# Kernel optimization log

Hardware: AMD Instinct MI355X
Metric: run time of the kernel (lower is better)

## Reference

```python
import jax, jax.numpy as jnp
import numpy as np

# BiAttn: additive (concat-based) cross attention.
# Original torch: e = Linear([k_i ; q_j]) = k_i @ W[:H] + q_j @ W[H:] + b  (separable)
# a = softmax(e, axis=-1 over Y); out[b,x,h] = sum_y v[b,y,h] * a[b,x,y]

B, X, Y, H = 8, 2048, 2048, 1024


def setup_inputs() -> dict:
    key = jax.random.key(0)
    kq, kk, kv, kw = jax.random.split(key, 4)
    q = jax.random.normal(kq, (B, Y, H), dtype=jnp.float32)
    k = jax.random.normal(kk, (B, X, H), dtype=jnp.float32)
    v = jax.random.normal(kv, (B, Y, H), dtype=jnp.float32)
    W = jax.random.normal(kw, (2 * H,), dtype=jnp.float32) * (1.0 / np.sqrt(2 * H))
    b = jnp.zeros((), dtype=jnp.float32)
    return {"q": q, "k": k, "v": v, "W": W, "b": b}


def reference(q, k, v, W, b):
    Hdim = k.shape[-1]
    Wk, Wq = W[:Hdim], W[Hdim:]
    # Separable additive score: e[b,x,y] = k[b,x]@Wk + q[b,y]@Wq + b
    sk = jnp.einsum('bxh,h->bx', k, Wk)          # [B, X]
    sq = jnp.einsum('byh,h->by', q, Wq)          # [B, Y]
    e = sk[:, :, None] + sq[:, None, :] + b      # [B, X, Y]
    a = jax.nn.softmax(e, axis=-1)               # softmax over Y
    out = jnp.einsum('byh,bxy->bxh', v, a)       # [B, X, H]
    return out
```

## Files before the change

### kernel.cpp

```cpp
#include <hip/hip_runtime.h>

#define Bn 8
#define Xn 2048
#define Yn 2048
#define Hn 1024
#define RPB 8
#define NPB (Yn / RPB)
#define YC 64
#define NCH (Yn / YC)


__global__ __launch_bounds__(256)
void k_pe(const float* __restrict__ q, const float* __restrict__ W,
          float* __restrict__ pe, float* __restrict__ sb,
          float* __restrict__ o) {
    const int blk = blockIdx.x;
    const int t = threadIdx.x;
    const int wave = t >> 6, lane = t & 63;
    __shared__ float ps[RPB];

    if (t == 0) ((float4*)o)[blk] = make_float4(0.f, 0.f, 0.f, 0.f);

    const float4* w4 = (const float4*)(W + Hn);
    const float4 ww0 = w4[lane];
    const float4 ww1 = w4[lane + 64];
    const float4 ww2 = w4[lane + 128];
    const float4 ww3 = w4[lane + 192];

    const int ra = blk * RPB + wave * 2;
    const float4* qa = (const float4*)(q + (size_t)ra * Hn);
    const float4* qb = qa + (Hn / 4);
    float acca = 0.f, accb = 0.f;
    #pragma unroll
    for (int i = 0; i < 4; ++i) {
        float4 a  = qa[lane + 64 * i];
        float4 bb = qb[lane + 64 * i];
        float4 w  = (i == 0) ? ww0 : (i == 1) ? ww1 : (i == 2) ? ww2 : ww3;
        acca += a.x * w.x + a.y * w.y + a.z * w.z + a.w * w.w;
        accb += bb.x * w.x + bb.y * w.y + bb.z * w.z + bb.w * w.w;
    }
    #pragma unroll
    for (int off = 32; off > 0; off >>= 1) {
        acca += __shfl_xor(acca, off, 64);
        accb += __shfl_xor(accb, off, 64);
    }
    if (lane == 0) {
        float ea = __expf(acca), eb = __expf(accb);
        pe[ra] = ea; pe[ra + 1] = eb;
        ps[wave * 2] = ea; ps[wave * 2 + 1] = eb;
    }
    __syncthreads();
    if (t == 0) {
        float s = 0.f;
        #pragma unroll
        for (int i = 0; i < RPB; ++i) s += ps[i];
        sb[blk] = s;
    }
}

__global__ __launch_bounds__(256)
void k_pv(const float* __restrict__ v, const float* __restrict__ pe,
          const float* __restrict__ sb, float* __restrict__ o) {
    const int b = blockIdx.y;
    const int c = blockIdx.x;
    const int y0 = c * YC;
    const int t = threadIdx.x;
    const int wave = t >> 6, lane = t & 63;
    __shared__ float wred[4];
    __shared__ float pw[YC];

    float s = sb[b * NPB + t];
    #pragma unroll
    for (int off = 32; off > 0; off >>= 1) s += __shfl_xor(s, off, 64);
    if (lane == 0) wred[wave] = s;
    __syncthreads();
    const float inv = 1.f / (wred[0] + wred[1] + wred[2] + wred[3]);

    if (t < YC) pw[t] = pe[b * Yn + y0 + t] * inv;
    __syncthreads();

    const float4* v4 = (const float4*)(v + ((size_t)b * Yn + y0) * Hn);
    float4 acc = {0.f, 0.f, 0.f, 0.f};
    #pragma unroll 16
    for (int yy = 0; yy < YC; ++yy) {
        const float p = pw[yy];
        const float4 vv = v4[(size_t)yy * (Hn / 4) + t];
        acc.x = fmaf(p, vv.x, acc.x);
        acc.y = fmaf(p, vv.y, acc.y);
        acc.z = fmaf(p, vv.z, acc.z);
        acc.w = fmaf(p, vv.w, acc.w);
    }
    float* ob = o + b * Hn + 4 * t;
    atomicAdd(ob + 0, acc.x);
    atomicAdd(ob + 1, acc.y);
    atomicAdd(ob + 2, acc.z);
    atomicAdd(ob + 3, acc.w);
}

__global__ void k_bcast(const float* __restrict__ o, float4* __restrict__ out) {
    const size_t i = (size_t)blockIdx.x * blockDim.x + threadIdx.x;
    const int h4 = (int)(i & (Hn / 4 - 1));
    const size_t row = i >> 8;
    const int b = (int)(row >> 11);
    const float4* o4 = (const float4*)o;
    out[i] = o4[b * (Hn / 4) + h4];
}

extern "C" void kernel_launch(void* const* d_in, const int* in_sizes, int n_in,
                              void* d_out, int out_size, void* d_ws, size_t ws_size,
                              hipStream_t stream) {
    const float* q = (const float*)d_in[0];
    const float* v = (const float*)d_in[2];
    const float* W = (const float*)d_in[3];
    float* out = (float*)d_out;

    float* pe = (float*)d_ws;
    float* sb = pe + (size_t)Bn * Yn;
    float* o  = sb + Bn * NPB;

    k_pe   <<<Bn * Yn / RPB, 256, 0, stream>>>(q, W, pe, sb, o);
    k_pv   <<<dim3(NCH, Bn), 256, 0, stream>>>(v, pe, sb, o);
    k_bcast<<<(Bn * (size_t)Xn * Hn / 4) / 256, 256, 0, stream>>>(o, (float4*)out);
}
```

Measured before the change: 203.7 us.

## Fuse score, PV and broadcast kernels into one cooperative kernel with grid syncs

Merges the three launches (score/exp, weighted V reduction, output broadcast) into a single cooperative kernel of 2048 blocks separated by two grid-wide barriers. The aim is to remove inter-kernel launch gaps and tail drain between stages. The kernel only runs cooperatively if occupancy allows every block to be co-resident; otherwise it falls back to the old three-kernel path. Grid syncs over many blocks add barrier cost, and the PV stage still runs on only a subset of the blocks.

```diff
diff --git a/kernel.cpp b/kernel.cpp
--- a/kernel.cpp
+++ b/kernel.cpp
@@ -1,4 +1,7 @@
 #include <hip/hip_runtime.h>
+#include <hip/hip_cooperative_groups.h>
+
+namespace cg = cooperative_groups;
 
 #define Bn 8
 #define Xn 2048
@@ -8,7 +11,107 @@
 #define NPB (Yn / RPB)
 #define YC 64
 #define NCH (Yn / YC)
-
+#define GRID (Bn * Yn / RPB)
+
+
+__global__ __launch_bounds__(256, 8)
+void k_all(const float* __restrict__ q, const float* __restrict__ W,
+           const float* __restrict__ v, float* __restrict__ pe,
+           float* __restrict__ sb, float* __restrict__ o,
+           float4* __restrict__ out) {
+    const int blk = blockIdx.x;
+    const int t = threadIdx.x;
+    const int wave = t >> 6, lane = t & 63;
+    __shared__ float ps[RPB];
+    __shared__ float wred[4];
+    __shared__ float pw[YC];
+
+    if (t == 0) ((float4*)o)[blk] = make_float4(0.f, 0.f, 0.f, 0.f);
+    {
+        const float4* w4 = (const float4*)(W + Hn);
+        const float4 ww0 = w4[lane];
+        const float4 ww1 = w4[lane + 64];
+        const float4 ww2 = w4[lane + 128];
+        const float4 ww3 = w4[lane + 192];
+
+        const int ra = blk * RPB + wave * 2;
+        const float4* qa = (const float4*)(q + (size_t)ra * Hn);
+        const float4* qb = qa + (Hn / 4);
+        float acca = 0.f, accb = 0.f;
+        #pragma unroll
+        for (int i = 0; i < 4; ++i) {
+            float4 a  = qa[lane + 64 * i];
+            float4 bb = qb[lane + 64 * i];
+            float4 w  = (i == 0) ? ww0 : (i == 1) ? ww1 : (i == 2) ? ww2 : ww3;
+            acca += a.x * w.x + a.y * w.y + a.z * w.z + a.w * w.w;
+            accb += bb.x * w.x + bb.y * w.y + bb.z * w.z + bb.w * w.w;
+        }
+        #pragma unroll
+        for (int off = 32; off > 0; off >>= 1) {
+            acca += __shfl_xor(acca, off, 64);
+            accb += __shfl_xor(accb, off, 64);
+        }
+        if (lane == 0) {
+            float ea = __expf(acca), eb = __expf(accb);
+            pe[ra] = ea; pe[ra + 1] = eb;
+            ps[wave * 2] = ea; ps[wave * 2 + 1] = eb;
+        }
+        __syncthreads();
+        if (t == 0) {
+            float s = 0.f;
+            #pragma unroll
+            for (int i = 0; i < RPB; ++i) s += ps[i];
+            sb[blk] = s;
+        }
+    }
+
+    cg::this_grid().sync();
+
+    if (blk < NCH * Bn) {
+        const int b = blk >> 5;
+        const int c = blk & (NCH - 1);
+        const int y0 = c * YC;
+
+        float s = sb[b * NPB + t];
+        #pragma unroll
+        for (int off = 32; off > 0; off >>= 1) s += __shfl_xor(s, off, 64);
+        if (lane == 0) wred[wave] = s;
+        __syncthreads();
+        const float inv = 1.f / (wred[0] + wred[1] + wred[2] + wred[3]);
+
+        if (t < YC) pw[t] = pe[b * Yn + y0 + t] * inv;
+        __syncthreads();
+
+        const float4* v4 = (const float4*)(v + ((size_t)b * Yn + y0) * Hn);
+        float4 acc = {0.f, 0.f, 0.f, 0.f};
+        #pragma unroll 16
+        for (int yy = 0; yy < YC; ++yy) {
+            const float p = pw[yy];
+            const float4 vv = v4[(size_t)yy * (Hn / 4) + t];
+            acc.x = fmaf(p, vv.x, acc.x);
+            acc.y = fmaf(p, vv.y, acc.y);
+            acc.z = fmaf(p, vv.z, acc.z);
+            acc.w = fmaf(p, vv.w, acc.w);
+        }
+        float* ob = o + b * Hn + 4 * t;
+        atomicAdd(ob + 0, acc.x);
+        atomicAdd(ob + 1, acc.y);
+        atomicAdd(ob + 2, acc.z);
+        atomicAdd(ob + 3, acc.w);
+    }
+
+    cg::this_grid().sync();
+
+    const float4* o4 = (const float4*)o;
+    #pragma unroll
+    for (int j = 0; j < 4; ++j) {
+        const size_t i = ((size_t)(blk * 4 + j)) * 256 + t;
+        const int h4 = (int)(i & (Hn / 4 - 1));
+        const size_t row = i >> 8;
+        const int b = (int)(row >> 11);
+        out[i] = o4[b * (Hn / 4) + h4];
+    }
+}
 
 __global__ __launch_bounds__(256)
 void k_pe(const float* __restrict__ q, const float* __restrict__ W,
@@ -18,15 +121,12 @@
     const int t = threadIdx.x;
     const int wave = t >> 6, lane = t & 63;
     __shared__ float ps[RPB];
-
     if (t == 0) ((float4*)o)[blk] = make_float4(0.f, 0.f, 0.f, 0.f);
-
     const float4* w4 = (const float4*)(W + Hn);
     const float4 ww0 = w4[lane];
     const float4 ww1 = w4[lane + 64];
     const float4 ww2 = w4[lane + 128];
     const float4 ww3 = w4[lane + 192];
-
     const int ra = blk * RPB + wave * 2;
     const float4* qa = (const float4*)(q + (size_t)ra * Hn);
     const float4* qb = qa + (Hn / 4);
@@ -68,17 +168,14 @@
     const int wave = t >> 6, lane = t & 63;
     __shared__ float wred[4];
     __shared__ float pw[YC];
-
     float s = sb[b * NPB + t];
     #pragma unroll
     for (int off = 32; off > 0; off >>= 1) s += __shfl_xor(s, off, 64);
     if (lane == 0) wred[wave] = s;
     __syncthreads();
     const float inv = 1.f / (wred[0] + wred[1] + wred[2] + wred[3]);
-
     if (t < YC) pw[t] = pe[b * Yn + y0 + t] * inv;
     __syncthreads();
-
     const float4* v4 = (const float4*)(v + ((size_t)b * Yn + y0) * Hn);
     float4 acc = {0.f, 0.f, 0.f, 0.f};
     #pragma unroll 16
@@ -118,7 +215,25 @@
     float* sb = pe + (size_t)Bn * Yn;
     float* o  = sb + Bn * NPB;
 
-    k_pe   <<<Bn * Yn / RPB, 256, 0, stream>>>(q, W, pe, sb, o);
-    k_pv   <<<dim3(NCH, Bn), 256, 0, stream>>>(v, pe, sb, o);
-    k_bcast<<<(Bn * (size_t)Xn * Hn / 4) / 256, 256, 0, stream>>>(o, (float4*)out);
-}
+    static int use_coop = -1;
+    if (use_coop < 0) {
+        int dev = 0, attr = 0, ncu = 0, nb = 0;
+        hipGetDevice(&dev);
+        hipDeviceGetAttribute(&attr, hipDeviceAttributeCooperativeLaunch, dev);
+        hipDeviceGetAttribute(&ncu, hipDeviceAttributeMultiprocessorCount, dev);
+        hipOccupancyMaxActiveBlocksPerMultiprocessor(&nb, k_all, 256, 0);
+        use_coop = (attr != 0 && nb * ncu >= GRID) ? 1 : 0;
+    }
+
+    if (use_coop) {
+        float4* out4 = (float4*)out;
+        void* args[] = {(void*)&q, (void*)&W, (void*)&v, (void*)&pe,
+                        (void*)&sb, (void*)&o, (void*)&out4};
+        hipLaunchCooperativeKernel((void*)k_all, dim3(GRID), dim3(256),
+                                   args, 0, stream);
+    } else {
+        k_pe   <<<GRID, 256, 0, stream>>>(q, W, pe, sb, o);
+        k_pv   <<<dim3(NCH, Bn), 256, 0, stream>>>(v, pe, sb, o);
+        k_bcast<<<(Bn * (size_t)Xn * Hn / 4) / 256, 256, 0, stream>>>(o, (float4*)out);
+    }
+}
```

Result: no change. 204.3 us (+0.3%).
